# Performance work log

Measured on AMD Instinct MI355X. Metric: run time of the kernel, lower is better.

## Reference

```python
import jax, jax.numpy as jnp
import numpy as np

TAU = 10.0
TOPK = 8
EPS = 1e-12


def _l2norm(x):
    return x / jnp.sqrt(jnp.sum(x * x, axis=-1, keepdims=True) + EPS)


def setup_inputs() -> dict:
    key = jax.random.key(0)
    k1, k2, k3, k4 = jax.random.split(key, 4)
    b, n, d_in, d_g, K = 4, 4096, 1024, 1024, 4096
    z = jax.random.normal(k1, (b, n, d_in), dtype=jnp.float32)
    target = jax.random.normal(k2, (b, n, d_g), dtype=jnp.float32)
    codebook = jax.random.normal(k3, (K, d_in), dtype=jnp.float32) / np.sqrt(d_in)
    E = jax.random.normal(k4, (K, d_g), dtype=jnp.float32) * 0.02
    return {"z": z, "target": target, "codebook": codebook, "E": E}


def reference(z, target, codebook, E):
    zf = _l2norm(z)            # [b,n,d_in]
    Cf = _l2norm(codebook)     # [K,d_in]
    logits = TAU * jnp.einsum('bnd,kd->bnk', zf, Cf)  # [b,n,K]
    vals, idx = jax.lax.top_k(logits, TOPK)           # [b,n,topk]
    alpha = jax.nn.softmax(vals, axis=-1)             # [b,n,topk]
    Ek = E[idx]                                       # [b,n,topk,d_g]
    g = jnp.sum(alpha[..., None] * Ek, axis=-2)       # [b,n,d_g]
    return target * (1.0 + g)
```

## Files before the change

### kernel.cpp

```cpp
#include <hip/hip_runtime.h>
#include <hip/hip_bf16.h>

#define M_ROWS 16384
#define D_DIM  1024
#define K_CB   4096

#define ZTILE  128
#define CTILE  256
#define NS     8
#define COLS_PER_SPLIT (K_CB / NS)
#define BODIES 32
#define MBLOCKS (M_ROWS / ZTILE)

typedef __attribute__((ext_vector_type(4))) int  int4v;
typedef __attribute__((ext_vector_type(8))) int  int8v;
typedef __attribute__((ext_vector_type(16))) float f32x16;

static __device__ __forceinline__ unsigned f2sortable(float f) {
  unsigned u = __float_as_uint(f);
  return (u & 0x80000000u) ? ~u : (u | 0x80000000u);
}

static __device__ __forceinline__ float sortable2f(unsigned s) {
  unsigned u = (s & 0x80000000u) ? (s ^ 0x80000000u) : ~s;
  return __uint_as_float(u);
}

static __device__ __forceinline__ unsigned char f2e4m3(float f) {
  float a = fabsf(f);
  const unsigned s = (__float_as_uint(f) >> 24) & 0x80u;
  if (a < 0.015625f) {
    int m = (int)(a * 512.0f + 0.5f);
    if (m >= 8) return (unsigned char)(s | 0x08u);
    return (unsigned char)(s | (unsigned)m);
  }
  if (a > 448.0f) a = 448.0f;
  unsigned t = __float_as_uint(a);
  t += 0x7FFFFu + ((t >> 20) & 1u);
  int e = (int)(t >> 23) - 127;
  unsigned m = (t >> 20) & 7u;
  if (e > 8 || (e == 8 && m == 7u)) { e = 8; m = 6u; }
  return (unsigned char)(s | ((unsigned)(e + 7) << 3) | m);
}

static __device__ __forceinline__ void gload_lds16(const unsigned char* g, unsigned char* l) {
  __builtin_amdgcn_global_load_lds(
      (const __attribute__((address_space(1))) void*)g,
      (__attribute__((address_space(3))) void*)l, 16, 0, 0);
}

__global__ __launch_bounds__(256)
void k_normalize(const float* __restrict__ z, const float* __restrict__ cb,
                 unsigned char* __restrict__ zf8, unsigned char* __restrict__ cbf8) {
  const int bid = blockIdx.x;
  const float* src;
  unsigned char* dst;
  if (bid < M_ROWS) {
    src = z + (size_t)bid * D_DIM;
    dst = zf8 + (size_t)bid * D_DIM;
  } else {
    const int r = bid - M_ROWS;
    src = cb + (size_t)r * D_DIM;
    dst = cbf8 + (size_t)r * D_DIM;
  }
  const int t = threadIdx.x;
  const float4 v = ((const float4*)src)[t];
  float ss = v.x * v.x + v.y * v.y + v.z * v.z + v.w * v.w;
#pragma unroll
  for (int off = 32; off > 0; off >>= 1) ss += __shfl_down(ss, off, 64);
  __shared__ float sp[4];
  if ((t & 63) == 0) sp[t >> 6] = ss;
  __syncthreads();
  const float tot = sp[0] + sp[1] + sp[2] + sp[3];
  const float sc = 16.0f / sqrtf(tot + 1e-12f);
  uchar4 o;
  o.x = f2e4m3(v.x * sc);
  o.y = f2e4m3(v.y * sc);
  o.z = f2e4m3(v.z * sc);
  o.w = f2e4m3(v.w * sc);
  *(uchar4*)(dst + 4 * t) = o;
}

__global__ __launch_bounds__(256, 2)
void k_gemm_topk(const unsigned char* __restrict__ zf8,
                 const unsigned char* __restrict__ cbf8,
                 unsigned* __restrict__ part) {
  __shared__ __align__(16) unsigned char smem[49152];

  const int tid  = threadIdx.x;
  const int lane = tid & 63;
  const int wid  = tid >> 6;
  const int wc   = wid & 1;
  const int wz   = wid >> 1;
  const int l31  = lane & 31;
  const int l5   = lane >> 5;

  const int wgid  = (int)blockIdx.x;
  const int split = wgid & 7;
  const int mtile = wgid >> 3;
  const int rbase = mtile * ZTILE;
  const int cbase = split * COLS_PER_SPLIT;

  int cA[4], zA[2];
#pragma unroll
  for (int mi = 0; mi < 4; ++mi) {
    const int r = wc * 128 + mi * 32 + l31;
    cA[mi] = r * 64 + (((2 * l5) ^ ((r >> 1) & 3)) << 4);
  }
#pragma unroll
  for (int nj = 0; nj < 2; ++nj) {
    const int r = wz * 64 + nj * 32 + l31;
    zA[nj] = r * 64 + (((2 * l5) ^ ((r >> 1) & 3)) << 4);
  }

  const long stoff = (long)(tid >> 2) * D_DIM + (((tid & 3) ^ ((tid >> 3) & 3)) << 4);
  const unsigned char* zsp = zf8 + (size_t)rbase * D_DIM + stoff;
  const unsigned char* csp = cbf8 + (size_t)cbase * D_DIM + stoff;

  f32x16 acc[4][2];
#pragma unroll
  for (int mi = 0; mi < 4; ++mi)
#pragma unroll
    for (int nj = 0; nj < 2; ++nj)
#pragma unroll
      for (int r = 0; r < 16; ++r) acc[mi][nj][r] = 0.f;

  unsigned tk[2][8];
#pragma unroll
  for (int l = 0; l < 2; ++l)
#pragma unroll
    for (int q = 0; q < 8; ++q) tk[l][q] = 0u;

  auto STAGE = [&](int par) {
    unsigned char* zd = smem + par * 8192 + tid * 16;
    unsigned char* cd = smem + 16384 + par * 16384 + tid * 16;
    gload_lds16(zsp,                zd);
    gload_lds16(zsp +  64 * D_DIM,  zd + 4096);
    gload_lds16(csp,                cd);
    gload_lds16(csp +  64 * D_DIM,  cd + 4096);
    gload_lds16(csp + 128 * D_DIM,  cd + 8192);
    gload_lds16(csp + 192 * D_DIM,  cd + 12288);
  };
  auto ADV = [&](int stagedBody) {
    if (((stagedBody + 1) & 15) == 0) {
      zsp += 64 - D_DIM;
      csp += 64 + (CTILE * D_DIM - D_DIM);
    } else {
      zsp += 64; csp += 64;
    }
  };
  auto COMPUTE = [&](int par) {
    const unsigned char* Z = smem + par * 8192;
    const unsigned char* C = smem + 16384 + par * 16384;
    int8v cf[4], zr[2];
#pragma unroll
    for (int mi = 0; mi < 4; ++mi) {
      ((int4v*)&cf[mi])[0] = *(const int4v*)(C + cA[mi]);
      ((int4v*)&cf[mi])[1] = *(const int4v*)(C + (cA[mi] ^ 16));
    }
#pragma unroll
    for (int nj = 0; nj < 2; ++nj) {
      ((int4v*)&zr[nj])[0] = *(const int4v*)(Z + zA[nj]);
      ((int4v*)&zr[nj])[1] = *(const int4v*)(Z + (zA[nj] ^ 16));
    }
    __builtin_amdgcn_s_setprio(1);
#pragma unroll
    for (int mi = 0; mi < 4; ++mi)
#pragma unroll
      for (int nj = 0; nj < 2; ++nj)
        acc[mi][nj] = __builtin_amdgcn_mfma_scale_f32_32x32x64_f8f6f4(
            cf[mi], zr[nj], acc[mi][nj],
            0 , 0 , 0, 0x7F, 0, 0x7F);
    __builtin_amdgcn_s_setprio(0);
  };
  auto EPILOGUE = [&](int chunk) {
    const int cfb0 = cbase + chunk * CTILE + wc * 128 + l5 * 4;
#pragma unroll
    for (int nj = 0; nj < 2; ++nj) {
#pragma unroll
      for (int mi = 0; mi < 4; ++mi) {
#pragma unroll
        for (int r = 0; r < 16; ++r) {
          const float v = acc[mi][nj][r];
          const unsigned idx = (unsigned)(cfb0 + mi * 32 + (r & 3) + ((r >> 2) << 3));
          const unsigned key = (f2sortable(v) & ~0xFFFu) | idx;
          if (key > tk[nj][0]) {
            unsigned cur = key;
#pragma unroll
            for (int q = 0; q < 7; ++q) {
              const unsigned a = tk[nj][q + 1];
              tk[nj][q] = (a < cur) ? a : cur;
              cur       = (a < cur) ? cur : a;
            }
            tk[nj][7] = cur;
          }
          acc[mi][nj][r] = 0.f;
        }
      }
    }
  };

  STAGE(0);
  ADV(0);
  __syncthreads();

  for (int b = 0; b < BODIES; b += 2) {
    STAGE(1);
    ADV(b + 1);
    COMPUTE(0);
    __syncthreads();

    if (b + 2 < BODIES) {
      STAGE(0);
      ADV(b + 2);
    }
    COMPUTE(1);
    if ((b & 15) == 14) EPILOGUE((b + 1) >> 4);
    __syncthreads();
  }

  unsigned* mrg = (unsigned*)smem;
  {
    const int slotw = (wc * 2 + l5) * 8;
#pragma unroll
    for (int nj = 0; nj < 2; ++nj) {
      const int zrow = wz * 64 + nj * 32 + l31;
#pragma unroll
      for (int q = 0; q < 8; ++q) mrg[zrow * 33 + slotw + q] = tk[nj][q];
    }
  }
  __syncthreads();
  if (tid < ZTILE) {
    const unsigned* c = mrg + tid * 33;
    unsigned top[8];
#pragma unroll
    for (int p = 0; p < 8; ++p) top[p] = 0u;
    unsigned tmin = 0u;
    for (int q0 = 0; q0 < 32; ++q0) {
      const unsigned k = c[(q0 + tid) & 31];
      if (k > tmin) {
        int ms = 0;
        unsigned mv = top[0];
#pragma unroll
        for (int q = 1; q < 8; ++q) { if (top[q] < mv) { mv = top[q]; ms = q; } }
#pragma unroll
        for (int q = 0; q < 8; ++q) top[q] = (q == ms) ? k : top[q];
        mv = top[0];
#pragma unroll
        for (int q = 1; q < 8; ++q) mv = (top[q] < mv) ? top[q] : mv;
        tmin = mv;
      }
    }
    unsigned* dst = part + ((size_t)(rbase + tid) * NS + split) * 8;
#pragma unroll
    for (int p = 0; p < 8; ++p) dst[p] = top[p];
  }
}

template<int NSP>
__global__ __launch_bounds__(256)
void k_gate(const unsigned* __restrict__ part, const float* __restrict__ target,
            const float* __restrict__ E, float* __restrict__ out) {
  constexpr int NK = NSP * 8;
  const int row = blockIdx.x;
  const int t = threadIdx.x;
  __shared__ float s_alpha[8];
  __shared__ int s_idx[8];
  __shared__ unsigned s_key[8];

  if (t < NK) {
    unsigned k = part[(size_t)row * NK + t];
#pragma unroll
    for (int p = 0; p < 8; ++p) {
      unsigned m = k;
#pragma unroll
      for (int off = NK / 2; off > 0; off >>= 1) {
        const unsigned o = __shfl_xor(m, off, NK);
        m = (m > o) ? m : o;
      }
      if (k == m) { s_key[p] = k; k = 0u; }
    }
  }
  __syncthreads();
  if (t < 8) {
    const float SCALE = 10.0f / 256.0f;
    const unsigned key = s_key[t];
    const float val  = SCALE * sortable2f(key & ~0xFFFu);
    const float vmax = SCALE * sortable2f(s_key[0] & ~0xFFFu);
    const float e = expf(val - vmax);
    float s = e;
#pragma unroll
    for (int off = 4; off > 0; off >>= 1) s += __shfl_xor(s, off, 8);
    s_alpha[t] = e / s;
    s_idx[t] = (int)(key & 0xFFFu);
  }
  __syncthreads();

  float4 g = {0.f, 0.f, 0.f, 0.f};
#pragma unroll
  for (int p = 0; p < 8; ++p) {
    const float a = s_alpha[p];
    const float4 e4 = ((const float4*)E)[(size_t)s_idx[p] * 256 + t];
    g.x += a * e4.x;
    g.y += a * e4.y;
    g.z += a * e4.z;
    g.w += a * e4.w;
  }
  const float4 tg = ((const float4*)target)[(size_t)row * 256 + t];
  float4 o;
  o.x = tg.x * (1.f + g.x);
  o.y = tg.y * (1.f + g.y);
  o.z = tg.z * (1.f + g.z);
  o.w = tg.w * (1.f + g.w);
  ((float4*)out)[(size_t)row * 256 + t] = o;
}

extern "C" void kernel_launch(void* const* d_in, const int* in_sizes, int n_in,
                              void* d_out, int out_size, void* d_ws, size_t ws_size,
                              hipStream_t stream) {
  const float* z      = (const float*)d_in[0];
  const float* target = (const float*)d_in[1];
  const float* cb     = (const float*)d_in[2];
  const float* E      = (const float*)d_in[3];
  float* out = (float*)d_out;

  unsigned char* zf8  = (unsigned char*)d_out;
  unsigned char* cbf8 = (unsigned char*)d_out + 16777216;
  unsigned* part = (unsigned*)d_ws;

  k_normalize<<<dim3(M_ROWS + K_CB), dim3(256), 0, stream>>>(z, cb, zf8, cbf8);
  k_gemm_topk<<<dim3(MBLOCKS * NS), dim3(256), 0, stream>>>(zf8, cbf8, part);
  k_gate<NS><<<dim3(M_ROWS), dim3(256), 0, stream>>>(part, target, E, out);
}
```

Measured before the change: 211.6 us.

## Triple-buffer FP8 GEMM LDS stages with vmcnt-based waits and single barrier

Replaces the double-buffered LDS pipeline with a three-slot ring in dynamic shared memory (72 KB), prefetching two bodies ahead. Each iteration reads its fragments, issues the next async global-to-LDS copy, runs the MFMAs, then waits with s_waitcnt vmcnt(6) and one raw barrier instead of two __syncthreads. The aim is to hide global load latency and cut barrier stalls. The larger LDS footprint may reduce occupancy below the two blocks per CU the launch bounds request.

```diff
diff --git a/kernel.cpp b/kernel.cpp
--- a/kernel.cpp
+++ b/kernel.cpp
@@ -11,6 +11,7 @@
 #define COLS_PER_SPLIT (K_CB / NS)
 #define BODIES 32
 #define MBLOCKS (M_ROWS / ZTILE)
+#define SLOT_B 24576
 
 typedef __attribute__((ext_vector_type(4))) int  int4v;
 typedef __attribute__((ext_vector_type(8))) int  int8v;
@@ -85,7 +86,7 @@
 void k_gemm_topk(const unsigned char* __restrict__ zf8,
                  const unsigned char* __restrict__ cbf8,
                  unsigned* __restrict__ part) {
-  __shared__ __align__(16) unsigned char smem[49152];
+  extern __shared__ __align__(16) unsigned char smem[];
 
   const int tid  = threadIdx.x;
   const int lane = tid & 63;
@@ -105,7 +106,7 @@
 #pragma unroll
   for (int mi = 0; mi < 4; ++mi) {
     const int r = wc * 128 + mi * 32 + l31;
-    cA[mi] = r * 64 + (((2 * l5) ^ ((r >> 1) & 3)) << 4);
+    cA[mi] = 8192 + r * 64 + (((2 * l5) ^ ((r >> 1) & 3)) << 4);
   }
 #pragma unroll
   for (int nj = 0; nj < 2; ++nj) {
@@ -131,9 +132,9 @@
 #pragma unroll
     for (int q = 0; q < 8; ++q) tk[l][q] = 0u;
 
-  auto STAGE = [&](int par) {
-    unsigned char* zd = smem + par * 8192 + tid * 16;
-    unsigned char* cd = smem + 16384 + par * 16384 + tid * 16;
+  auto STAGE_AT = [&](int dstBase) {
+    unsigned char* zd = smem + dstBase + tid * 16;
+    unsigned char* cd = smem + dstBase + 8192 + tid * 16;
     gload_lds16(zsp,                zd);
     gload_lds16(zsp +  64 * D_DIM,  zd + 4096);
     gload_lds16(csp,                cd);
@@ -149,30 +150,6 @@
       zsp += 64; csp += 64;
     }
   };
-  auto COMPUTE = [&](int par) {
-    const unsigned char* Z = smem + par * 8192;
-    const unsigned char* C = smem + 16384 + par * 16384;
-    int8v cf[4], zr[2];
-#pragma unroll
-    for (int mi = 0; mi < 4; ++mi) {
-      ((int4v*)&cf[mi])[0] = *(const int4v*)(C + cA[mi]);
-      ((int4v*)&cf[mi])[1] = *(const int4v*)(C + (cA[mi] ^ 16));
-    }
-#pragma unroll
-    for (int nj = 0; nj < 2; ++nj) {
-      ((int4v*)&zr[nj])[0] = *(const int4v*)(Z + zA[nj]);
-      ((int4v*)&zr[nj])[1] = *(const int4v*)(Z + (zA[nj] ^ 16));
-    }
-    __builtin_amdgcn_s_setprio(1);
-#pragma unroll
-    for (int mi = 0; mi < 4; ++mi)
-#pragma unroll
-      for (int nj = 0; nj < 2; ++nj)
-        acc[mi][nj] = __builtin_amdgcn_mfma_scale_f32_32x32x64_f8f6f4(
-            cf[mi], zr[nj], acc[mi][nj],
-            0 , 0 , 0, 0x7F, 0, 0x7F);
-    __builtin_amdgcn_s_setprio(0);
-  };
   auto EPILOGUE = [&](int chunk) {
     const int cfb0 = cbase + chunk * CTILE + wc * 128 + l5 * 4;
 #pragma unroll
@@ -200,25 +177,58 @@
     }
   };
 
-  STAGE(0);
-  ADV(0);
-  __syncthreads();
-
-  for (int b = 0; b < BODIES; b += 2) {
-    STAGE(1);
-    ADV(b + 1);
-    COMPUTE(0);
-    __syncthreads();
+  STAGE_AT(0);          ADV(0);
+  STAGE_AT(SLOT_B);     ADV(1);
+  asm volatile("s_waitcnt vmcnt(6)" ::: "memory");
+  __builtin_amdgcn_s_barrier();
+  __builtin_amdgcn_sched_barrier(0);
+
+  int slotBase = 0;
+  int sdBase   = 2 * SLOT_B;
+  for (int b = 0; b < BODIES; ++b) {
+    const unsigned char* S = smem + slotBase;
+    int8v cf[4], zr[2];
+#pragma unroll
+    for (int mi = 0; mi < 4; ++mi) {
+      ((int4v*)&cf[mi])[0] = *(const int4v*)(S + cA[mi]);
+      ((int4v*)&cf[mi])[1] = *(const int4v*)(S + (cA[mi] ^ 16));
+    }
+#pragma unroll
+    for (int nj = 0; nj < 2; ++nj) {
+      ((int4v*)&zr[nj])[0] = *(const int4v*)(S + zA[nj]);
+      ((int4v*)&zr[nj])[1] = *(const int4v*)(S + (zA[nj] ^ 16));
+    }
 
     if (b + 2 < BODIES) {
-      STAGE(0);
+      STAGE_AT(sdBase);
       ADV(b + 2);
     }
-    COMPUTE(1);
-    if ((b & 15) == 14) EPILOGUE((b + 1) >> 4);
-    __syncthreads();
-  }
-
+
+    __builtin_amdgcn_s_setprio(1);
+#pragma unroll
+    for (int mi = 0; mi < 4; ++mi)
+#pragma unroll
+      for (int nj = 0; nj < 2; ++nj)
+        acc[mi][nj] = __builtin_amdgcn_mfma_scale_f32_32x32x64_f8f6f4(
+            cf[mi], zr[nj], acc[mi][nj],
+            0 , 0 , 0, 0x7F, 0, 0x7F);
+    __builtin_amdgcn_s_setprio(0);
+
+    if (b == 15) EPILOGUE(0);
+
+    if (b + 2 < BODIES)       asm volatile("s_waitcnt vmcnt(6)" ::: "memory");
+    else if (b + 1 < BODIES)  asm volatile("s_waitcnt vmcnt(0)" ::: "memory");
+    if (b + 1 < BODIES) {
+      __builtin_amdgcn_s_barrier();
+      __builtin_amdgcn_sched_barrier(0);
+    }
+
+    slotBase += (slotBase < 2 * SLOT_B) ? SLOT_B : -2 * SLOT_B;
+    sdBase   += (sdBase   < 2 * SLOT_B) ? SLOT_B : -2 * SLOT_B;
+  }
+  EPILOGUE(1);
+
+  __syncthreads();
   unsigned* mrg = (unsigned*)smem;
   {
     const int slotw = (wc * 2 + l5) * 8;
@@ -328,7 +338,10 @@
   unsigned char* cbf8 = (unsigned char*)d_out + 16777216;
   unsigned* part = (unsigned*)d_ws;
 
+  hipFuncSetAttribute((const void*)k_gemm_topk,
+                      hipFuncAttributeMaxDynamicSharedMemorySize, 73728);
+
   k_normalize<<<dim3(M_ROWS + K_CB), dim3(256), 0, stream>>>(z, cb, zf8, cbf8);
-  k_gemm_topk<<<dim3(MBLOCKS * NS), dim3(256), 0, stream>>>(zf8, cbf8, part);
+  k_gemm_topk<<<dim3(MBLOCKS * NS), dim3(256), 73728, stream>>>(zf8, cbf8, part);
   k_gate<NS><<<dim3(M_ROWS), dim3(256), 0, stream>>>(part, target, E, out);
 }
```

Measured after the change: 313.9 us. 1.48x slower.
